# Kernel tuning notes

Measured on AMD Instinct MI355X. Metric: run time of the kernel, lower is better.

## Reference

```python
import jax, jax.numpy as jnp
import numpy as np

T, B, OBS, ENC, H, A = 128, 256, 512, 256, 512, 18
N = T * B


def setup_inputs() -> dict:
    key = jax.random.key(0)
    ks = jax.random.split(key, 16)
    s = 0.02
    return {
        "x": jax.random.normal(ks[0], (N, OBS), jnp.float32),
        "gru_state": jax.random.normal(ks[1], (1, B, H), jnp.float32),
        "done": (jax.random.uniform(ks[2], (N,)) < 0.05).astype(jnp.float32),
        "action": jax.random.randint(ks[3], (N,), 0, A),
        # encoder MLP
        "w1": jax.random.normal(ks[4], (ENC, OBS), jnp.float32) * s,
        "b1": jnp.zeros((ENC,), jnp.float32),
        "w2": jax.random.normal(ks[5], (ENC, ENC), jnp.float32) * s,
        "b2": jnp.zeros((ENC,), jnp.float32),
        # GRU (PyTorch layout: gates [r, z, n] stacked along dim 0)
        "w_ih": jax.random.normal(ks[6], (3 * H, ENC), jnp.float32) * s,
        "w_hh": jax.random.normal(ks[7], (3 * H, H), jnp.float32) * s,
        "b_ih": jnp.zeros((3 * H,), jnp.float32),
        "b_hh": jnp.zeros((3 * H,), jnp.float32),
        # heads
        "w_actor": jax.random.normal(ks[8], (A, H), jnp.float32) * 0.01,
        "b_actor": jnp.zeros((A,), jnp.float32),
        "w_critic": jax.random.normal(ks[9], (1, H), jnp.float32) * s,
        "b_critic": jnp.zeros((1,), jnp.float32),
    }


def _gru_agent(x, gru_state, done, action, w1, b1, w2, b2, w_ih, w_hh, b_ih, b_hh,
               w_actor, b_actor, w_critic, b_critic):
    # MLP encoder
    h = jax.nn.relu(x @ w1.T + b1)
    h = jax.nn.relu(h @ w2.T + b2)  # (N, ENC)
    b = gru_state.shape[1]
    hs = h.reshape(-1, b, h.shape[-1])      # (T, B, ENC)
    dn = done.reshape(-1, b)                # (T, B)
    # precompute input-side gates for all timesteps: (T, B, 3H)
    gx = jnp.einsum('tbi,gi->tbg', hs, w_ih) + b_ih

    def step(h_prev, inp):
        gx_t, d_t = inp
        h_prev = h_prev * (1.0 - d_t)[:, None]   # done-based reset
        gh = h_prev @ w_hh.T + b_hh
        xr, xz, xn = jnp.split(gx_t, 3, axis=-1)
        hr, hz, hn = jnp.split(gh, 3, axis=-1)
        r = jax.nn.sigmoid(xr + hr)
        z = jax.nn.sigmoid(xz + hz)
        n = jnp.tanh(xn + r * hn)
        h_new = (1.0 - z) * n + z * h_prev
        return h_new, h_new

    h_last, outs = jax.lax.scan(step, gru_state[0], (gx, dn))
    hidden = outs.reshape(-1, outs.shape[-1])   # (N, H)

    logits = hidden @ w_actor.T + b_actor
    logp = jax.nn.log_softmax(logits, axis=-1)
    log_prob = jnp.take_along_axis(logp, action[:, None], axis=1)[:, 0]
    entropy = -jnp.sum(jnp.exp(logp) * logp, axis=-1)
    value = hidden @ w_critic.T + b_critic       # (N, 1)
    return log_prob, entropy, value, h_last[None]


def reference(x, gru_state, done, action, w1, b1, w2, b2, w_ih, w_hh, b_ih, b_hh,
              w_actor, b_actor, w_critic, b_critic):
    return _gru_agent(x, gru_state, done, action, w1, b1, w2, b2, w_ih, w_hh,
                      b_ih, b_hh, w_actor, b_actor, w_critic, b_critic)
```

## Files before the change

### kernel.cpp

```cpp
#include <hip/hip_runtime.h>
#include <hip/hip_bf16.h>

typedef short bf16x8 __attribute__((ext_vector_type(8)));
typedef float f32x4 __attribute__((ext_vector_type(4)));
typedef unsigned short u16;
typedef unsigned int u32;
typedef unsigned long long u64;

#define AS1 __attribute__((address_space(1)))
#define AS3 __attribute__((address_space(3)))

__device__ __forceinline__ u16 f2bf(float f) {
    __hip_bfloat16 h = __float2bfloat16(f);
    u16 r;
    __builtin_memcpy(&r, &h, 2);
    return r;
}
__device__ __forceinline__ float bf2f(u16 u) {
    u32 v = ((u32)u) << 16;
    float f;
    __builtin_memcpy(&f, &v, 4);
    return f;
}


constexpr int NW1  = 256 * 512;
constexpr int NW2  = 256 * 256;
constexpr int NWIH = 1536 * 256;

__global__ __launch_bounds__(256) void prep_kernel(
    const float* __restrict__ w1, const float* __restrict__ w2,
    const float* __restrict__ wih, const float* __restrict__ wact,
    const float* __restrict__ wcrit,
    u16* __restrict__ w1b, u16* __restrict__ w2b,
    u16* __restrict__ wihb, u16* __restrict__ wcatb) {
    long long gid = (long long)blockIdx.x * 256 + threadIdx.x;
    long long i4 = gid * 4;
    const float* src;
    u16* dst;
    if (i4 < NW1) { src = w1; dst = w1b; }
    else if ((i4 -= NW1) < NW2) { src = w2; dst = w2b; }
    else if ((i4 -= NW2) < NWIH) { src = wih; dst = wihb; }
    else {
        i4 -= NWIH;
        #pragma unroll
        for (int e = 0; e < 4; e++) {
            long long idx = i4 + e;
            int row = (int)(idx >> 9), col = (int)(idx & 511);
            float v = (row < 18) ? wact[row * 512 + col]
                    : (row == 18 ? wcrit[col] : 0.f);
            wcatb[idx] = f2bf(v);
        }
        return;
    }
    float4 v = *reinterpret_cast<const float4*>(src + i4);
    uint2 p;
    p.x = (u32)f2bf(v.x) | ((u32)f2bf(v.y) << 16);
    p.y = (u32)f2bf(v.z) | ((u32)f2bf(v.w) << 16);
    *reinterpret_cast<uint2*>(dst + i4) = p;
}

__global__ __launch_bounds__(256) void gemm_a32_bt_kernel(
    const float* __restrict__ A, const u16* __restrict__ B,
    const float* __restrict__ bias, u16* __restrict__ out,
    int M, int N, int K) {
    __shared__ u16 As[128 * 64];
    __shared__ u16 Bs[128 * 64];
    int tid = threadIdx.x;
    int lane = tid & 63, wave = tid >> 6;
    int m16 = lane & 15, quad = lane >> 4;
    int nb = N >> 7;
    int bm = blockIdx.x / nb, bn = blockIdx.x % nb;
    int wm = wave >> 1, wn = wave & 1;

    f32x4 acc[4][4];
    #pragma unroll
    for (int i = 0; i < 4; i++)
        #pragma unroll
        for (int j = 0; j < 4; j++) acc[i][j] = (f32x4){0.f, 0.f, 0.f, 0.f};

    const int rbase = wave * 32 + (lane >> 3);
    const int cpr = lane & 7;
    const int ar = tid >> 1, ah = (tid & 1) * 32;
    int kiters = K >> 6;
    for (int kb = 0; kb < kiters; kb++) {
        #pragma unroll
        for (int i = 0; i < 4; i++) {
            int r = rbase + i * 8;
            int cg = cpr ^ (r & 7);
            const u16* gb_ = B + (long long)(bn * 128 + r) * K + kb * 64 + cg * 8;
            __builtin_amdgcn_global_load_lds((const AS1 u32*)gb_, (AS3 u32*)&Bs[r * 64 + cpr * 8], 16, 0, 0);
        }
        const float* ga = A + (long long)(bm * 128 + ar) * K + kb * 64 + ah;
        #pragma unroll
        for (int g = 0; g < 4; g++) {
            float4 v0 = *reinterpret_cast<const float4*>(ga + g * 8);
            float4 v1 = *reinterpret_cast<const float4*>(ga + g * 8 + 4);
            uint4 pk;
            pk.x = (u32)f2bf(v0.x) | ((u32)f2bf(v0.y) << 16);
            pk.y = (u32)f2bf(v0.z) | ((u32)f2bf(v0.w) << 16);
            pk.z = (u32)f2bf(v1.x) | ((u32)f2bf(v1.y) << 16);
            pk.w = (u32)f2bf(v1.z) | ((u32)f2bf(v1.w) << 16);
            int sc = ((ah >> 3) + g) ^ (ar & 7);
            *reinterpret_cast<uint4*>(&As[ar * 64 + sc * 8]) = pk;
        }
        __syncthreads();
        #pragma unroll
        for (int ks = 0; ks < 2; ks++) {
            bf16x8 af[4], bfr[4];
            int lc = ks * 4 + quad;
            #pragma unroll
            for (int mt = 0; mt < 4; mt++) {
                int m = wm * 64 + mt * 16 + m16;
                af[mt] = *reinterpret_cast<const bf16x8*>(&As[m * 64 + (lc ^ (m & 7)) * 8]);
            }
            #pragma unroll
            for (int nt = 0; nt < 4; nt++) {
                int n = wn * 64 + nt * 16 + m16;
                bfr[nt] = *reinterpret_cast<const bf16x8*>(&Bs[n * 64 + (lc ^ (n & 7)) * 8]);
            }
            #pragma unroll
            for (int mt = 0; mt < 4; mt++)
                #pragma unroll
                for (int nt = 0; nt < 4; nt++)
                    acc[mt][nt] = __builtin_amdgcn_mfma_f32_16x16x32_bf16(af[mt], bfr[nt], acc[mt][nt], 0, 0, 0);
        }
        __syncthreads();
    }
    #pragma unroll
    for (int nt = 0; nt < 4; nt++) {
        int n = bn * 128 + wn * 64 + nt * 16 + m16;
        float bv = bias[n];
        #pragma unroll
        for (int mt = 0; mt < 4; mt++) {
            #pragma unroll
            for (int i = 0; i < 4; i++) {
                int m = bm * 128 + wm * 64 + mt * 16 + quad * 4 + i;
                float v = acc[mt][nt][i] + bv;
                out[(long long)m * N + n] = f2bf(fmaxf(v, 0.f));
            }
        }
    }
}

__global__ __launch_bounds__(256) void gemm_bt_kernel(
    const u16* __restrict__ A, const u16* __restrict__ B,
    const float* __restrict__ bias, u16* __restrict__ out,
    int M, int N, int K, int mode) {
    __shared__ u16 As[128 * 64];
    __shared__ u16 Bs[128 * 64];
    int tid = threadIdx.x;
    int lane = tid & 63, wave = tid >> 6;
    int m16 = lane & 15, quad = lane >> 4;
    int nb = N >> 7;
    int bm = blockIdx.x / nb, bn = blockIdx.x % nb;
    int wm = wave >> 1, wn = wave & 1;

    f32x4 acc[4][4];
    #pragma unroll
    for (int i = 0; i < 4; i++)
        #pragma unroll
        for (int j = 0; j < 4; j++) acc[i][j] = (f32x4){0.f, 0.f, 0.f, 0.f};

    const int rbase = wave * 32 + (lane >> 3);
    const int cpr = lane & 7;
    int kiters = K >> 6;
    for (int kb = 0; kb < kiters; kb++) {
        #pragma unroll
        for (int i = 0; i < 4; i++) {
            int r = rbase + i * 8;
            int cg = cpr ^ (r & 7);
            const u16* ga = A + (long long)(bm * 128 + r) * K + kb * 64 + cg * 8;
            const u16* gb_ = B + (long long)(bn * 128 + r) * K + kb * 64 + cg * 8;
            __builtin_amdgcn_global_load_lds((const AS1 u32*)ga, (AS3 u32*)&As[r * 64 + cpr * 8], 16, 0, 0);
            __builtin_amdgcn_global_load_lds((const AS1 u32*)gb_, (AS3 u32*)&Bs[r * 64 + cpr * 8], 16, 0, 0);
        }
        __syncthreads();
        #pragma unroll
        for (int ks = 0; ks < 2; ks++) {
            bf16x8 af[4], bfr[4];
            int lc = ks * 4 + quad;
            #pragma unroll
            for (int mt = 0; mt < 4; mt++) {
                int m = wm * 64 + mt * 16 + m16;
                af[mt] = *reinterpret_cast<const bf16x8*>(&As[m * 64 + (lc ^ (m & 7)) * 8]);
            }
            #pragma unroll
            for (int nt = 0; nt < 4; nt++) {
                int n = wn * 64 + nt * 16 + m16;
                bfr[nt] = *reinterpret_cast<const bf16x8*>(&Bs[n * 64 + (lc ^ (n & 7)) * 8]);
            }
            #pragma unroll
            for (int mt = 0; mt < 4; mt++)
                #pragma unroll
                for (int nt = 0; nt < 4; nt++)
                    acc[mt][nt] = __builtin_amdgcn_mfma_f32_16x16x32_bf16(af[mt], bfr[nt], acc[mt][nt], 0, 0, 0);
        }
        __syncthreads();
    }
    if (mode == 0) {
        #pragma unroll
        for (int nt = 0; nt < 4; nt++) {
            int n = bn * 128 + wn * 64 + nt * 16 + m16;
            float bv = bias[n];
            #pragma unroll
            for (int mt = 0; mt < 4; mt++) {
                #pragma unroll
                for (int i = 0; i < 4; i++) {
                    int m = bm * 128 + wm * 64 + mt * 16 + quad * 4 + i;
                    float v = acc[mt][nt][i] + bv;
                    out[(long long)m * N + n] = f2bf(fmaxf(v, 0.f));
                }
            }
        }
    } else {
        #pragma unroll
        for (int nt = 0; nt < 4; nt++) {
            int n = bn * 128 + wn * 64 + nt * 16 + m16;
            float bv = bias[n];
            int gkind = n >> 9, gj = n & 511;
            int gu = gj >> 5;
            int gate_local = gkind * 32 + (gj & 31);
            #pragma unroll
            for (int mt = 0; mt < 4; mt++) {
                #pragma unroll
                for (int i = 0; i < 4; i++) {
                    int m = bm * 128 + wm * 64 + mt * 16 + quad * 4 + i;
                    int t = m >> 8, bg = m & 255;
                    long long dst = ((((long long)t * 16 + (bg >> 4)) * 16 + gu) * 16 + (bg & 15)) * 96 + gate_local;
                    out[dst] = f2bf(acc[mt][nt][i] + bv);
                }
            }
        }
    }
}

__global__ __launch_bounds__(256) void scan_kernel(
    const float* __restrict__ gru_state, const float* __restrict__ done,
    const float* __restrict__ w_hh, const float* __restrict__ b_hh,
    const u16* __restrict__ gx, u64* h_pub, u16* hidden,
    float* h_last) {
    __shared__ float partial[2][4][16][98];
    int tid = threadIdx.x;
    int lane = tid & 63, wave = tid >> 6;
    int m16 = lane & 15, quad = lane >> 4;
    int gb = blockIdx.x & 15, gu = blockIdx.x >> 4;

    bf16x8 wfrag[6][4];
    #pragma unroll
    for (int nt = 0; nt < 6; nt++) {
        int g = nt * 16 + m16;
        int row = (g >> 5) * 512 + gu * 32 + (g & 31);
        #pragma unroll
        for (int ks = 0; ks < 4; ks++) {
            int k0 = wave * 128 + ks * 32 + quad * 8;
            const float* wp = w_hh + row * 512 + k0;
            float4 v0 = *reinterpret_cast<const float4*>(wp);
            float4 v1 = *reinterpret_cast<const float4*>(wp + 4);
            bf16x8 f;
            f[0] = (short)f2bf(v0.x); f[1] = (short)f2bf(v0.y);
            f[2] = (short)f2bf(v0.z); f[3] = (short)f2bf(v0.w);
            f[4] = (short)f2bf(v1.x); f[5] = (short)f2bf(v1.y);
            f[6] = (short)f2bf(v1.z); f[7] = (short)f2bf(v1.w);
            wfrag[nt][ks] = f;
        }
    }
    int b_ = tid >> 4, jj = (tid & 15) * 2;
    int bglob = gb * 16 + b_;
    int unit = gu * 32 + jj;
    float bhr0 = b_hh[unit],        bhr1 = b_hh[unit + 1];
    float bhz0 = b_hh[512 + unit],  bhz1 = b_hh[512 + unit + 1];
    float bhn0 = b_hh[1024 + unit], bhn1 = b_hh[1024 + unit + 1];
    float hs0 = gru_state[bglob * 512 + unit];
    float hs1 = gru_state[bglob * 512 + unit + 1];

    {
        u32 p = (u32)f2bf(hs0) | ((u32)f2bf(hs1) << 16);
        u64 pub = ((u64)1 << 32) | (u64)p;
        __hip_atomic_store(h_pub + (size_t)bglob * 256 + (unit >> 1), pub,
                           __ATOMIC_RELAXED, __HIP_MEMORY_SCOPE_AGENT);
    }

    const size_t rowoff = (size_t)(gb * 16 + m16) * 256 + (size_t)wave * 64 + quad * 4;

    for (int t = 0; t < 128; t++) {
        const u16* gxp = gx + ((size_t)((t * 16 + gb) * 16 + gu) * 16 + b_) * 96;
        u32 pr = *reinterpret_cast<const u32*>(gxp + jj);
        u32 pz = *reinterpret_cast<const u32*>(gxp + 32 + jj);
        u32 pn = *reinterpret_cast<const u32*>(gxp + 64 + jj);
        float grx = bf2f((u16)pr), gry = bf2f((u16)(pr >> 16));
        float gzx = bf2f((u16)pz), gzy = bf2f((u16)(pz >> 16));
        float gnx = bf2f((u16)pn), gny = bf2f((u16)(pn >> 16));
        float dne = done[t * 256 + bglob];
        float dnr = done[t * 256 + gb * 16 + m16];

        u64* rowp = h_pub + (size_t)(t & 1) * 65536 + rowoff;
        u64 e[4][4];
        const u32 want = (u32)(t + 1);
        for (;;) {
            #pragma unroll
            for (int ks = 0; ks < 4; ks++)
                #pragma unroll
                for (int j = 0; j < 4; j++)
                    e[ks][j] = __hip_atomic_load(rowp + ks * 16 + j,
                                                 __ATOMIC_RELAXED, __HIP_MEMORY_SCOPE_AGENT);
            int mine = 1;
            #pragma unroll
            for (int ks = 0; ks < 4; ks++)
                #pragma unroll
                for (int j = 0; j < 4; j++)
                    mine &= ((u32)(e[ks][j] >> 32) == want);
            if (__all(mine)) break;
        }
        bool zrow = dnr >= 0.5f;
        bf16x8 af[4];
        #pragma unroll
        for (int ks = 0; ks < 4; ks++) {
            union { u32 w[4]; bf16x8 v; } u;
            #pragma unroll
            for (int j = 0; j < 4; j++) u.w[j] = zrow ? 0u : (u32)e[ks][j];
            af[ks] = u.v;
        }
        f32x4 acc[6];
        #pragma unroll
        for (int nt = 0; nt < 6; nt++) acc[nt] = (f32x4){0.f, 0.f, 0.f, 0.f};
        #pragma unroll
        for (int ks = 0; ks < 4; ks++)
            #pragma unroll
            for (int nt = 0; nt < 6; nt++)
                acc[nt] = __builtin_amdgcn_mfma_f32_16x16x32_bf16(af[ks], wfrag[nt][ks], acc[nt], 0, 0, 0);
        #pragma unroll
        for (int nt = 0; nt < 6; nt++)
            #pragma unroll
            for (int i = 0; i < 4; i++)
                partial[t & 1][wave][quad * 4 + i][nt * 16 + m16] = acc[nt][i];
        __syncthreads();
        float sr0 = 0, sr1 = 0, sz0 = 0, sz1 = 0, sn0 = 0, sn1 = 0;
        #pragma unroll
        for (int w = 0; w < 4; w++) {
            const float* p = &partial[t & 1][w][b_][0];
            float2 a0 = *reinterpret_cast<const float2*>(p + jj);
            float2 a1 = *reinterpret_cast<const float2*>(p + 32 + jj);
            float2 a2 = *reinterpret_cast<const float2*>(p + 64 + jj);
            sr0 += a0.x; sr1 += a0.y;
            sz0 += a1.x; sz1 += a1.y;
            sn0 += a2.x; sn1 += a2.y;
        }
        float scale = 1.f - dne;
        hs0 *= scale; hs1 *= scale;
        float r0 = 1.f / (1.f + __expf(-(grx + sr0 + bhr0)));
        float r1 = 1.f / (1.f + __expf(-(gry + sr1 + bhr1)));
        float z0 = 1.f / (1.f + __expf(-(gzx + sz0 + bhz0)));
        float z1 = 1.f / (1.f + __expf(-(gzy + sz1 + bhz1)));
        float pn0 = gnx + r0 * (sn0 + bhn0);
        float pn1 = gny + r1 * (sn1 + bhn1);
        float n0 = 1.f - 2.f / (__expf(2.f * pn0) + 1.f);
        float n1 = 1.f - 2.f / (__expf(2.f * pn1) + 1.f);
        hs0 = (1.f - z0) * n0 + z0 * hs0;
        hs1 = (1.f - z1) * n1 + z1 * hs1;
        u32 packed = (u32)f2bf(hs0) | ((u32)f2bf(hs1) << 16);
        if (t < 127) {
            u64 pub = ((u64)(u32)(t + 2) << 32) | (u64)packed;
            __hip_atomic_store(h_pub + (size_t)((t + 1) & 1) * 65536 +
                               (size_t)bglob * 256 + (unit >> 1), pub,
                               __ATOMIC_RELAXED, __HIP_MEMORY_SCOPE_AGENT);
        } else {
            h_last[bglob * 512 + unit] = hs0;
            h_last[bglob * 512 + unit + 1] = hs1;
        }
        ((u32*)hidden)[((long long)(t * 256 + bglob) * 512 + unit) / 2] = packed;
    }
}

__global__ __launch_bounds__(256) void heads_kernel(
    const u16* __restrict__ hidden, const u16* __restrict__ wcat,
    const float* __restrict__ b_actor, const float* __restrict__ b_critic,
    const int* __restrict__ action, float* __restrict__ out) {
    __shared__ float cls[4][16][34];
    int tid = threadIdx.x, lane = tid & 63, wave = tid >> 6;
    int m16 = lane & 15, quad = lane >> 4;
    int r0 = (blockIdx.x * 4 + wave) * 16;
    f32x4 acc0 = (f32x4){0.f, 0.f, 0.f, 0.f}, acc1 = (f32x4){0.f, 0.f, 0.f, 0.f};
    #pragma unroll
    for (int ks = 0; ks < 16; ks++) {
        bf16x8 a = *reinterpret_cast<const bf16x8*>(&hidden[(long long)(r0 + m16) * 512 + ks * 32 + quad * 8]);
        bf16x8 b0 = *reinterpret_cast<const bf16x8*>(&wcat[m16 * 512 + ks * 32 + quad * 8]);
        bf16x8 b1 = *reinterpret_cast<const bf16x8*>(&wcat[(16 + m16) * 512 + ks * 32 + quad * 8]);
        acc0 = __builtin_amdgcn_mfma_f32_16x16x32_bf16(a, b0, acc0, 0, 0, 0);
        acc1 = __builtin_amdgcn_mfma_f32_16x16x32_bf16(a, b1, acc1, 0, 0, 0);
    }
    #pragma unroll
    for (int i = 0; i < 4; i++) {
        cls[wave][quad * 4 + i][m16] = acc0[i];
        cls[wave][quad * 4 + i][16 + m16] = acc1[i];
    }
    __syncthreads();
    if (lane < 16) {
        int row = r0 + lane;
        float lg[18];
        float mx = -1e30f;
        #pragma unroll
        for (int a2 = 0; a2 < 18; a2++) {
            lg[a2] = cls[wave][lane][a2] + b_actor[a2];
            mx = fmaxf(mx, lg[a2]);
        }
        float s = 0.f, sl = 0.f;
        #pragma unroll
        for (int a2 = 0; a2 < 18; a2++) {
            float e = __expf(lg[a2] - mx);
            s += e; sl += e * lg[a2];
        }
        float logZ = mx + __logf(s);
        int act = action[row];
        float la = 0.f;
        #pragma unroll
        for (int a2 = 0; a2 < 18; a2++)
            if (a2 == act) la = lg[a2];
        out[row] = la - logZ;
        out[32768 + row] = logZ - sl / s;
        out[65536 + row] = cls[wave][lane][18] + b_critic[0];
    }
}

extern "C" void kernel_launch(void* const* d_in, const int* in_sizes, int n_in,
                              void* d_out, int out_size, void* d_ws, size_t ws_size,
                              hipStream_t stream) {
    const float* x        = (const float*)d_in[0];
    const float* gru_st   = (const float*)d_in[1];
    const float* done     = (const float*)d_in[2];
    const int*   action   = (const int*)d_in[3];
    const float* w1       = (const float*)d_in[4];
    const float* b1       = (const float*)d_in[5];
    const float* w2       = (const float*)d_in[6];
    const float* b2       = (const float*)d_in[7];
    const float* w_ih     = (const float*)d_in[8];
    const float* w_hh     = (const float*)d_in[9];
    const float* b_ih     = (const float*)d_in[10];
    const float* b_hh     = (const float*)d_in[11];
    const float* w_actor  = (const float*)d_in[12];
    const float* b_actor  = (const float*)d_in[13];
    const float* w_critic = (const float*)d_in[14];
    const float* b_critic = (const float*)d_in[15];
    float* out = (float*)d_out;

    char* ws = (char*)d_ws;
    u16* h1     = (u16*)(ws + 0LL);
    u16* h2     = (u16*)(ws + 16777216LL);
    u16* hidden = (u16*)(ws + 0LL);
    u16* w1b    = (u16*)(ws + 33554432LL);
    u16* w2b    = (u16*)(ws + 33816576LL);
    u16* wihb   = (u16*)(ws + 33947648LL);
    u16* wcatb  = (u16*)(ws + 34734080LL);
    u64* h_pub  = (u64*)(ws + 34766848LL);
    u16* gxb    = (u16*)(ws + 37748736LL);
    float* h_last = out + 3 * 32768;

    prep_kernel<<<592, 256, 0, stream>>>(w1, w2, w_ih, w_actor, w_critic,
                                         w1b, w2b, wihb, wcatb);
    gemm_a32_bt_kernel<<<512, 256, 0, stream>>>(x, w1b, b1, h1, 32768, 256, 512);
    gemm_bt_kernel<<<512, 256, 0, stream>>>(h1, w2b, b2, h2, 32768, 256, 256, 0);
    gemm_bt_kernel<<<3072, 256, 0, stream>>>(h2, wihb, b_ih, gxb, 32768, 1536, 256, 1);

    void* args[] = {(void*)&gru_st, (void*)&done, (void*)&w_hh, (void*)&b_hh,
                    (void*)&gxb, (void*)&h_pub, (void*)&hidden, (void*)&h_last};
    hipLaunchCooperativeKernel((void*)scan_kernel, dim3(256), dim3(256), args, 0, stream);

    heads_kernel<<<512, 256, 0, stream>>>(hidden, wcatb, b_actor, b_critic, action, out);
}
```

Baseline: 761.9 us.

## Replace per-element versioned hidden-state publishing with per-wave flag counters

The scan kernel used to publish each hidden-state pair as a 64-bit word carrying a step tag, and consumers spun on loading and checking every tagged word. Now producers store plain 32-bit packed state, wait for their stores to complete, and then have lane 0 of each wave bump a per-wave flag. Consumers spin on 64 flags for their batch group and then read the state once with wide loads. This halves the traffic of published state and removes the repeated polling of data words, at the cost of an extra store-completion wait and flag write per step. The ordering relies on relaxed atomics plus s_waitcnt rather than release/acquire semantics. The double-buffered partial shared-memory array is also reduced to a single buffer.

```diff
diff --git a/kernel.cpp b/kernel.cpp
--- a/kernel.cpp
+++ b/kernel.cpp
@@ -238,9 +238,9 @@
 __global__ __launch_bounds__(256) void scan_kernel(
     const float* __restrict__ gru_state, const float* __restrict__ done,
     const float* __restrict__ w_hh, const float* __restrict__ b_hh,
-    const u16* __restrict__ gx, u64* h_pub, u16* hidden,
+    const u16* __restrict__ gx, u32* h_pub, u32* flags, u16* hidden,
     float* h_last) {
-    __shared__ float partial[2][4][16][98];
+    __shared__ float partial[4][16][98];
     int tid = threadIdx.x;
     int lane = tid & 63, wave = tid >> 6;
     int m16 = lane & 15, quad = lane >> 4;
@@ -276,12 +276,15 @@
 
     {
         u32 p = (u32)f2bf(hs0) | ((u32)f2bf(hs1) << 16);
-        u64 pub = ((u64)1 << 32) | (u64)p;
-        __hip_atomic_store(h_pub + (size_t)bglob * 256 + (unit >> 1), pub,
+        __hip_atomic_store(h_pub + (size_t)bglob * 256 + (unit >> 1), p,
                            __ATOMIC_RELAXED, __HIP_MEMORY_SCOPE_AGENT);
     }
-
-    const size_t rowoff = (size_t)(gb * 16 + m16) * 256 + (size_t)wave * 64 + quad * 4;
+    __builtin_amdgcn_s_waitcnt(0x0f70);
+    if (lane == 0)
+        __hip_atomic_store(&flags[gb * 64 + gu * 4 + wave], 1u,
+                           __ATOMIC_RELAXED, __HIP_MEMORY_SCOPE_AGENT);
+
+    const size_t fragoff = (size_t)(gb * 16 + m16) * 256 + (size_t)wave * 64 + quad * 4;
 
     for (int t = 0; t < 128; t++) {
         const u16* gxp = gx + ((size_t)((t * 16 + gb) * 16 + gu) * 16 + b_) * 96;
@@ -294,31 +297,24 @@
         float dne = done[t * 256 + bglob];
         float dnr = done[t * 256 + gb * 16 + m16];
 
-        u64* rowp = h_pub + (size_t)(t & 1) * 65536 + rowoff;
-        u64 e[4][4];
         const u32 want = (u32)(t + 1);
-        for (;;) {
-            #pragma unroll
-            for (int ks = 0; ks < 4; ks++)
-                #pragma unroll
-                for (int j = 0; j < 4; j++)
-                    e[ks][j] = __hip_atomic_load(rowp + ks * 16 + j,
-                                                 __ATOMIC_RELAXED, __HIP_MEMORY_SCOPE_AGENT);
-            int mine = 1;
-            #pragma unroll
-            for (int ks = 0; ks < 4; ks++)
-                #pragma unroll
-                for (int j = 0; j < 4; j++)
-                    mine &= ((u32)(e[ks][j] >> 32) == want);
-            if (__all(mine)) break;
+        while (__hip_atomic_load(&flags[gb * 64 + lane],
+                                 __ATOMIC_RELAXED, __HIP_MEMORY_SCOPE_AGENT) < want) {}
+
+        const u64* hp = (const u64*)(h_pub + (size_t)(t & 1) * 65536 + fragoff);
+        u64 e[4][2];
+        #pragma unroll
+        for (int ks = 0; ks < 4; ks++) {
+            e[ks][0] = __hip_atomic_load(hp + ks * 8, __ATOMIC_RELAXED, __HIP_MEMORY_SCOPE_AGENT);
+            e[ks][1] = __hip_atomic_load(hp + ks * 8 + 1, __ATOMIC_RELAXED, __HIP_MEMORY_SCOPE_AGENT);
         }
         bool zrow = dnr >= 0.5f;
         bf16x8 af[4];
         #pragma unroll
         for (int ks = 0; ks < 4; ks++) {
-            union { u32 w[4]; bf16x8 v; } u;
-            #pragma unroll
-            for (int j = 0; j < 4; j++) u.w[j] = zrow ? 0u : (u32)e[ks][j];
+            union { u64 d[2]; bf16x8 v; } u;
+            u.d[0] = zrow ? 0ull : e[ks][0];
+            u.d[1] = zrow ? 0ull : e[ks][1];
             af[ks] = u.v;
         }
         f32x4 acc[6];
@@ -333,12 +329,12 @@
         for (int nt = 0; nt < 6; nt++)
             #pragma unroll
             for (int i = 0; i < 4; i++)
-                partial[t & 1][wave][quad * 4 + i][nt * 16 + m16] = acc[nt][i];
+                partial[wave][quad * 4 + i][nt * 16 + m16] = acc[nt][i];
         __syncthreads();
         float sr0 = 0, sr1 = 0, sz0 = 0, sz1 = 0, sn0 = 0, sn1 = 0;
         #pragma unroll
         for (int w = 0; w < 4; w++) {
-            const float* p = &partial[t & 1][w][b_][0];
+            const float* p = &partial[w][b_][0];
             float2 a0 = *reinterpret_cast<const float2*>(p + jj);
             float2 a1 = *reinterpret_cast<const float2*>(p + 32 + jj);
             float2 a2 = *reinterpret_cast<const float2*>(p + 64 + jj);
@@ -359,16 +355,19 @@
         hs0 = (1.f - z0) * n0 + z0 * hs0;
         hs1 = (1.f - z1) * n1 + z1 * hs1;
         u32 packed = (u32)f2bf(hs0) | ((u32)f2bf(hs1) << 16);
+        ((u32*)hidden)[(size_t)(t * 256 + bglob) * 256 + (unit >> 1)] = packed;
         if (t < 127) {
-            u64 pub = ((u64)(u32)(t + 2) << 32) | (u64)packed;
             __hip_atomic_store(h_pub + (size_t)((t + 1) & 1) * 65536 +
-                               (size_t)bglob * 256 + (unit >> 1), pub,
+                               (size_t)bglob * 256 + (unit >> 1), packed,
                                __ATOMIC_RELAXED, __HIP_MEMORY_SCOPE_AGENT);
+            __builtin_amdgcn_s_waitcnt(0x0f70);
+            if (lane == 0)
+                __hip_atomic_store(&flags[gb * 64 + gu * 4 + wave], (u32)(t + 2),
+                                   __ATOMIC_RELAXED, __HIP_MEMORY_SCOPE_AGENT);
         } else {
             h_last[bglob * 512 + unit] = hs0;
             h_last[bglob * 512 + unit + 1] = hs1;
         }
-        ((u32*)hidden)[((long long)(t * 256 + bglob) * 512 + unit) / 2] = packed;
     }
 }
 
@@ -451,10 +450,12 @@
     u16* w2b    = (u16*)(ws + 33816576LL);
     u16* wihb   = (u16*)(ws + 33947648LL);
     u16* wcatb  = (u16*)(ws + 34734080LL);
-    u64* h_pub  = (u64*)(ws + 34766848LL);
+    u32* h_pub  = (u32*)(ws + 34766848LL);
+    u32* flags  = (u32*)(ws + 35291136LL);
     u16* gxb    = (u16*)(ws + 37748736LL);
     float* h_last = out + 3 * 32768;
 
+    hipMemsetAsync(flags, 0, 16 * 64 * 4, stream);
     prep_kernel<<<592, 256, 0, stream>>>(w1, w2, w_ih, w_actor, w_critic,
                                          w1b, w2b, wihb, wcatb);
     gemm_a32_bt_kernel<<<512, 256, 0, stream>>>(x, w1b, b1, h1, 32768, 256, 512);
@@ -462,7 +463,8 @@
     gemm_bt_kernel<<<3072, 256, 0, stream>>>(h2, wihb, b_ih, gxb, 32768, 1536, 256, 1);
 
     void* args[] = {(void*)&gru_st, (void*)&done, (void*)&w_hh, (void*)&b_hh,
-                    (void*)&gxb, (void*)&h_pub, (void*)&hidden, (void*)&h_last};
+                    (void*)&gxb, (void*)&h_pub, (void*)&flags, (void*)&hidden,
+                    (void*)&h_last};
     hipLaunchCooperativeKernel((void*)scan_kernel, dim3(256), dim3(256), args, 0, stream);
 
     heads_kernel<<<512, 256, 0, stream>>>(hidden, wcatb, b_actor, b_critic, action, out);
```

Result: slower. 1.010 ms (+32.6%).
